# Kernel optimization log

Hardware: AMD Instinct MI355X
Metric: run time of the kernel (lower is better)

The kernel has to match this reference:

```python
import jax, jax.numpy as jnp
import numpy as np

N = 100000      # nodes
E = 1600000     # edges (before self-loops)
IN_C = 128
HID = 256
L = 4
EPS = 1e-5


def setup_inputs() -> dict:
    key = jax.random.key(0)
    ks = jax.random.split(key, 12)
    s = 0.05
    x = jax.random.normal(ks[0], (N, IN_C), dtype=jnp.float32)
    edge_index = jax.random.randint(ks[1], (2, E), 0, N, dtype=jnp.int64)
    enc_w = jax.random.normal(ks[2], (IN_C, HID), dtype=jnp.float32) * s
    enc_b = jnp.zeros((HID,), jnp.float32)
    conv_w = jax.random.normal(ks[3], (L, HID, HID), dtype=jnp.float32) * s
    conv_b = jnp.zeros((L, HID), jnp.float32)
    ln_g = jnp.ones((L, HID), jnp.float32)
    ln_b = jnp.zeros((L, HID), jnp.float32)
    lin1_w = jax.random.normal(ks[4], (HID, HID // 2), dtype=jnp.float32) * s
    lin1_b = jnp.zeros((HID // 2,), jnp.float32)
    lin2_w = jax.random.normal(ks[5], (HID // 2, 1), dtype=jnp.float32) * s
    lin2_b = jnp.zeros((1,), jnp.float32)
    return dict(x=x, edge_index=edge_index, enc_w=enc_w, enc_b=enc_b,
                conv_w=conv_w, conv_b=conv_b, ln_g=ln_g, ln_b=ln_b,
                lin1_w=lin1_w, lin1_b=lin1_b, lin2_w=lin2_w, lin2_b=lin2_b)


def _layer_norm(h, g, b):
    mu = jnp.mean(h, axis=-1, keepdims=True)
    var = jnp.mean(jnp.square(h - mu), axis=-1, keepdims=True)
    return (h - mu) * jax.lax.rsqrt(var + EPS) * g + b


def reference(x, edge_index, enc_w, enc_b, conv_w, conv_b, ln_g, ln_b,
              lin1_w, lin1_b, lin2_w, lin2_b):
    loops = jnp.arange(N, dtype=edge_index.dtype)
    row = jnp.concatenate([edge_index[0], loops])   # source
    col = jnp.concatenate([edge_index[1], loops])   # target
    # GCN symmetric norm with self-loop weight 1 (improved=False)
    deg = jax.ops.segment_sum(jnp.ones(row.shape[0], jnp.float32), col,
                              num_segments=N)
    dis = jnp.where(deg > 0, jax.lax.rsqrt(deg), 0.0)  # deg^-1/2, [N]

    h = x @ enc_w + enc_b
    for i in range(L):
        hw = h @ conv_w[i]
        # norm_e = dis[row]*dis[col]: scale at source, aggregate, scale at target
        agg = jax.ops.segment_sum((hw * dis[:, None])[row], col,
                                  num_segments=N)
        h = agg * dis[:, None] + conv_b[i]
        h = jax.nn.relu(_layer_norm(h, ln_g[i], ln_b[i]))
        # dropout p=0.1 is identity in eval mode
    h = jax.nn.relu(h @ lin1_w + lin1_b)
    return h @ lin2_w + lin2_b  # [N, 1]
```

## Files before the change

### kernel.cpp

```cpp
#include <hip/hip_runtime.h>

#define N_NODES 100000
#define N_EDGES 1600000
#define IN_C    128
#define HID     256
#define NLAYER  4

#define NBUCK 391
#define BCAP  8192
#define EPB   4096
#define CAPL  6144

typedef __attribute__((ext_vector_type(8))) __bf16 bf16x8;
typedef __attribute__((ext_vector_type(4))) float  floatx4;

__device__ inline unsigned short f2b(float f) {
    unsigned u = __builtin_bit_cast(unsigned, f);
    return (unsigned short)((u + 0x7fffu + ((u >> 16) & 1u)) >> 16);
}
__device__ inline float b2f(unsigned short s) {
    unsigned u = ((unsigned)s) << 16;
    return __builtin_bit_cast(float, u);
}
__device__ inline void acc8(float* a, uint4 v) {
    unsigned wds[4] = {v.x, v.y, v.z, v.w};
    #pragma unroll
    for (int k = 0; k < 4; ++k) {
        a[2*k]   += __builtin_bit_cast(float, wds[k] << 16);
        a[2*k+1] += __builtin_bit_cast(float, wds[k] & 0xffff0000u);
    }
}

__global__ void kb_zero(int* g, int m) {
    int i = blockIdx.x * blockDim.x + threadIdx.x;
    if (i < m) g[i] = 0;
}

__global__ __launch_bounds__(256) void kb_scatter(
        const int* __restrict__ row, const int* __restrict__ col,
        int* __restrict__ gfill, uint2* __restrict__ pairs, int e) {
    __shared__ uint2 ep[EPB];
    __shared__ int hist[NBUCK];
    __shared__ int lbase[NBUCK];
    const int tid  = threadIdx.x;
    const int base = blockIdx.x * EPB;
    for (int b = tid; b < NBUCK; b += 256) hist[b] = 0;
    __syncthreads();
    #pragma unroll
    for (int k = 0; k < EPB / 256; ++k) {
        int i = base + k * 256 + tid;
        uint2 pr = make_uint2(0xffffffffu, 0u);
        if (i < e) {
            pr.x = (unsigned)col[i];
            pr.y = (unsigned)row[i];
            atomicAdd(&hist[pr.x >> 8], 1);
        }
        ep[k * 256 + tid] = pr;
    }
    __syncthreads();
    for (int b = tid; b < NBUCK; b += 256) {
        int h = hist[b];
        lbase[b] = h ? atomicAdd(&gfill[b], h) : 0;
    }
    __syncthreads();
    for (int b = tid; b < NBUCK; b += 256) hist[b] = 0;
    __syncthreads();
    #pragma unroll
    for (int k = 0; k < EPB / 256; ++k) {
        uint2 pr = ep[k * 256 + tid];
        if (pr.x != 0xffffffffu) {
            int bk = pr.x >> 8;
            int p  = lbase[bk] + atomicAdd(&hist[bk], 1);
            if (p < BCAP) pairs[(size_t)bk * BCAP + p] = pr;
        }
    }
}

__global__ void kb_scan(const int* __restrict__ gfill, int* __restrict__ boff,
                        int* __restrict__ offs) {
    __shared__ int wsum[8];
    const int t = threadIdx.x, lane = t & 63, w = t >> 6;
    int v = (t < NBUCK) ? gfill[t] : 0;
    int inc = v;
    #pragma unroll
    for (int o = 1; o < 64; o <<= 1) { int u = __shfl_up(inc, o); if (lane >= o) inc += u; }
    if (lane == 63) wsum[w] = inc;
    __syncthreads();
    if (t == 0) { int r = 0; for (int i = 0; i < 8; ++i) { int x = wsum[i]; wsum[i] = r; r += x; } }
    __syncthreads();
    int excl = wsum[w] + inc - v;
    if (t <= NBUCK) boff[t] = excl;
    if (t == 0) offs[N_NODES] = N_EDGES;
}

__global__ __launch_bounds__(256) void kb_build(
        const uint2* __restrict__ pairs, const int* __restrict__ gfill,
        const int* __restrict__ boff,
        int* __restrict__ offs, float* __restrict__ dis,
        int* __restrict__ srcl, int n) {
    __shared__ int lcnt[256];
    __shared__ int lstart[256];
    __shared__ int wsum[4];
    __shared__ int sl[CAPL];
    const int b = blockIdx.x;
    const int tid = threadIdx.x, lane = tid & 63, w = tid >> 6;
    int cnt = gfill[b]; if (cnt > CAPL) cnt = CAPL;
    const int base = boff[b];
    const uint2* bp = pairs + (size_t)b * BCAP;
    lcnt[tid] = 0;
    __syncthreads();
    for (int i = tid; i < cnt; i += 256)
        atomicAdd(&lcnt[bp[i].x & 255], 1);
    __syncthreads();
    int v = lcnt[tid];
    int inc = v;
    #pragma unroll
    for (int o = 1; o < 64; o <<= 1) { int u = __shfl_up(inc, o); if (lane >= o) inc += u; }
    if (lane == 63) wsum[w] = inc;
    __syncthreads();
    if (tid == 0) { int r = 0; for (int i = 0; i < 4; ++i) { int x = wsum[i]; wsum[i] = r; r += x; } }
    __syncthreads();
    int excl = wsum[w] + inc - v;
    lstart[tid] = excl;
    int node = (b << 8) + tid;
    if (node < n) {
        dis[node]  = rsqrtf((float)(v + 1));
        offs[node] = base + excl;
    }
    __syncthreads();
    lcnt[tid] = 0;
    __syncthreads();
    for (int i = tid; i < cnt; i += 256) {
        uint2 pr = bp[i];
        int c = pr.x & 255;
        int q = lstart[c] + atomicAdd(&lcnt[c], 1);
        sl[q] = (int)pr.y;
    }
    __syncthreads();
    for (int i = tid; i < cnt; i += 256)
        srcl[base + i] = sl[i];
}

__global__ void k_f2b4(const float* __restrict__ src, unsigned short* __restrict__ dst, int n4) {
    int i = blockIdx.x * blockDim.x + threadIdx.x;
    if (i < n4) {
        float4 v = ((const float4*)src)[i];
        ushort4 o;
        o.x = f2b(v.x); o.y = f2b(v.y); o.z = f2b(v.z); o.w = f2b(v.w);
        ((ushort4*)dst)[i] = o;
    }
}

__global__ void k_wt(const float* __restrict__ W, unsigned short* __restrict__ Wt, int K, int Nn) {
    int idx = blockIdx.x * blockDim.x + threadIdx.x;
    if (idx < K * Nn) {
        int k = idx / Nn, n = idx % Nn;
        Wt[n * K + k] = f2b(W[idx]);
    }
}

template<int MODE>
__global__ __launch_bounds__(256) void k_mm(
        const unsigned short* __restrict__ A,
        const unsigned short* __restrict__ Wt,
        const float* __restrict__ bias, const float* __restrict__ scale,
        void* __restrict__ Cout, int M, int K, int Nn) {
    __shared__ unsigned short As[128 * 32];
    __shared__ unsigned short Bs[128 * 32];
    const int tid  = threadIdx.x;
    const int lane = tid & 63;
    const int w    = tid >> 6;
    const int bm   = blockIdx.x * 128;
    const int bn   = blockIdx.y * 128;

    const int i0 = tid, i1 = tid + 256;
    const int r0 = i0 >> 2, r1 = i1 >> 2;
    const int q0 = i0 & 3,  q1 = i1 & 3;
    const int a_off0 = min(bm + r0, M - 1) * K + q0 * 8;
    const int a_off1 = min(bm + r1, M - 1) * K + q1 * 8;
    const int b_off0 = (bn + r0) * K + q0 * 8;
    const int b_off1 = (bn + r1) * K + q1 * 8;

    uint4 ra0, ra1, rb0, rb1;
    floatx4 acc[4][4];
    #pragma unroll
    for (int i = 0; i < 4; ++i)
        #pragma unroll
        for (int j = 0; j < 4; ++j)
            acc[i][j] = (floatx4){0.f, 0.f, 0.f, 0.f};

    const int wm = (w & 1) * 64;
    const int wn = (w >> 1) * 64;
    const int fm = lane & 15;
    const int fq = (lane >> 4) * 8;

    ra0 = *(const uint4*)(A  + a_off0);
    ra1 = *(const uint4*)(A  + a_off1);
    rb0 = *(const uint4*)(Wt + b_off0);
    rb1 = *(const uint4*)(Wt + b_off1);

    const int KT = K >> 5;
    for (int kt = 0; kt < KT; ++kt) {
        ((uint4*)As)[i0] = ra0; ((uint4*)As)[i1] = ra1;
        ((uint4*)Bs)[i0] = rb0; ((uint4*)Bs)[i1] = rb1;
        __syncthreads();
        if (kt + 1 < KT) {
            int k0 = (kt + 1) << 5;
            ra0 = *(const uint4*)(A  + a_off0 + k0);
            ra1 = *(const uint4*)(A  + a_off1 + k0);
            rb0 = *(const uint4*)(Wt + b_off0 + k0);
            rb1 = *(const uint4*)(Wt + b_off1 + k0);
        }
        bf16x8 af[4], bfr[4];
        #pragma unroll
        for (int i = 0; i < 4; ++i)
            af[i] = *(const bf16x8*)(const void*)(As + (wm + i * 16 + fm) * 32 + fq);
        #pragma unroll
        for (int j = 0; j < 4; ++j)
            bfr[j] = *(const bf16x8*)(const void*)(Bs + (wn + j * 16 + fm) * 32 + fq);
        #pragma unroll
        for (int i = 0; i < 4; ++i)
            #pragma unroll
            for (int j = 0; j < 4; ++j)
                acc[i][j] = __builtin_amdgcn_mfma_f32_16x16x32_bf16(af[i], bfr[j], acc[i][j], 0, 0, 0);
        __syncthreads();
    }

    const int quad = lane >> 4;
    #pragma unroll
    for (int i = 0; i < 4; ++i) {
        #pragma unroll
        for (int r = 0; r < 4; ++r) {
            int row = bm + wm + i * 16 + quad * 4 + r;
            if (row >= M) continue;
            float sc = scale ? scale[row] : 1.f;
            #pragma unroll
            for (int j = 0; j < 4; ++j) {
                int colg = bn + wn + j * 16 + fm;
                float v = acc[i][j][r];
                if (MODE == 0) v += bias[colg];
                v *= sc;
                ((unsigned short*)Cout)[(size_t)row * Nn + colg] = f2b(v);
            }
        }
    }
}

__global__ __launch_bounds__(256) void k_head(
        const unsigned short* __restrict__ A,
        const unsigned short* __restrict__ Wt,
        const float* __restrict__ b1, const float* __restrict__ w2,
        const float* __restrict__ b2, float* __restrict__ out, int M) {
    const int K = 256;
    __shared__ unsigned short As[128 * 32];
    __shared__ unsigned short Bs[128 * 32];
    const int tid  = threadIdx.x;
    const int lane = tid & 63;
    const int w    = tid >> 6;
    const int bm   = blockIdx.x * 128;

    const int i0 = tid, i1 = tid + 256;
    const int r0 = i0 >> 2, r1 = i1 >> 2;
    const int q0 = i0 & 3,  q1 = i1 & 3;
    const int a_off0 = min(bm + r0, M - 1) * K + q0 * 8;
    const int a_off1 = min(bm + r1, M - 1) * K + q1 * 8;
    const int b_off0 = r0 * K + q0 * 8;
    const int b_off1 = r1 * K + q1 * 8;

    uint4 ra0, ra1, rb0, rb1;
    floatx4 acc[4][4];
    #pragma unroll
    for (int i = 0; i < 4; ++i)
        #pragma unroll
        for (int j = 0; j < 4; ++j)
            acc[i][j] = (floatx4){0.f, 0.f, 0.f, 0.f};

    const int wm = (w & 1) * 64;
    const int wn = (w >> 1) * 64;
    const int fm = lane & 15;
    const int fq = (lane >> 4) * 8;

    ra0 = *(const uint4*)(A  + a_off0);
    ra1 = *(const uint4*)(A  + a_off1);
    rb0 = *(const uint4*)(Wt + b_off0);
    rb1 = *(const uint4*)(Wt + b_off1);

    for (int kt = 0; kt < 8; ++kt) {
        ((uint4*)As)[i0] = ra0; ((uint4*)As)[i1] = ra1;
        ((uint4*)Bs)[i0] = rb0; ((uint4*)Bs)[i1] = rb1;
        __syncthreads();
        if (kt + 1 < 8) {
            int k0 = (kt + 1) << 5;
            ra0 = *(const uint4*)(A  + a_off0 + k0);
            ra1 = *(const uint4*)(A  + a_off1 + k0);
            rb0 = *(const uint4*)(Wt + b_off0 + k0);
            rb1 = *(const uint4*)(Wt + b_off1 + k0);
        }
        bf16x8 af[4], bfr[4];
        #pragma unroll
        for (int i = 0; i < 4; ++i)
            af[i] = *(const bf16x8*)(const void*)(As + (wm + i * 16 + fm) * 32 + fq);
        #pragma unroll
        for (int j = 0; j < 4; ++j)
            bfr[j] = *(const bf16x8*)(const void*)(Bs + (wn + j * 16 + fm) * 32 + fq);
        #pragma unroll
        for (int i = 0; i < 4; ++i)
            #pragma unroll
            for (int j = 0; j < 4; ++j)
                acc[i][j] = __builtin_amdgcn_mfma_f32_16x16x32_bf16(af[i], bfr[j], acc[i][j], 0, 0, 0);
        __syncthreads();
    }

    float* red = (float*)As;
    const int q = lane >> 4;
    float b1v[4], w2v[4];
    #pragma unroll
    for (int j = 0; j < 4; ++j) {
        int col = wn + j * 16 + fm;
        b1v[j] = b1[col]; w2v[j] = w2[col];
    }
    #pragma unroll
    for (int i = 0; i < 4; ++i) {
        #pragma unroll
        for (int r = 0; r < 4; ++r) {
            float s = 0.f;
            #pragma unroll
            for (int j = 0; j < 4; ++j)
                s += fmaxf(acc[i][j][r] + b1v[j], 0.f) * w2v[j];
            #pragma unroll
            for (int off = 1; off < 16; off <<= 1) s += __shfl_xor(s, off);
            if (fm == 0) {
                int m = wm + i * 16 + q * 4 + r;
                red[m * 2 + (wn >> 6)] = s;
            }
        }
    }
    __syncthreads();
    if (tid < 128) {
        int row = bm + tid;
        if (row < M) out[row] = red[tid * 2] + red[tid * 2 + 1] + b2[0];
    }
}

__global__ void k_agg(const unsigned short* __restrict__ hw, const int* __restrict__ srcl,
                      const int* __restrict__ offs, const float* __restrict__ dis,
                      const float* __restrict__ cb, const float* __restrict__ g,
                      const float* __restrict__ bt, unsigned short* __restrict__ hout, int n) {
    int gtid = blockIdx.x * blockDim.x + threadIdx.x;
    int node = __builtin_amdgcn_readfirstlane(gtid >> 6);
    int lane = threadIdx.x & 63;
    const int half = lane >> 5;
    const int sub  = lane & 31;
    const uint4* T = (const uint4*)hw;

    float a[8] = {0,0,0,0,0,0,0,0};
    float c[8] = {0,0,0,0,0,0,0,0};
    if (half == 0) {
        uint4 v = T[(size_t)node * 32 + sub];
        acc8(a, v);
    }
    int p = offs[node], pe = offs[node + 1];
    for (; p + 7 < pe; p += 8) {
        int s0 = srcl[p],     s1 = srcl[p + 1], s2 = srcl[p + 2], s3 = srcl[p + 3];
        int s4 = srcl[p + 4], s5 = srcl[p + 5], s6 = srcl[p + 6], s7 = srcl[p + 7];
        int ea = half ? s1 : s0;
        int eb = half ? s3 : s2;
        int ec = half ? s5 : s4;
        int ed = half ? s7 : s6;
        uint4 va = T[(size_t)ea * 32 + sub];
        uint4 vb = T[(size_t)eb * 32 + sub];
        uint4 vc = T[(size_t)ec * 32 + sub];
        uint4 vd = T[(size_t)ed * 32 + sub];
        acc8(a, va);
        acc8(c, vb);
        acc8(a, vc);
        acc8(c, vd);
    }
    for (; p + 1 < pe; p += 2) {
        int s0 = srcl[p], s1 = srcl[p + 1];
        int ea = half ? s1 : s0;
        uint4 v = T[(size_t)ea * 32 + sub];
        acc8(a, v);
    }
    if (p < pe && half == 0) {
        int s0 = srcl[p];
        uint4 v = T[(size_t)s0 * 32 + sub];
        acc8(a, v);
    }
    #pragma unroll
    for (int j = 0; j < 8; ++j) {
        a[j] += c[j];
        a[j] += __shfl_xor(a[j], 32);
    }
    float dc = dis[node];
    const float4* cb4 = (const float4*)cb;
    const float4* g4  = (const float4*)g;
    const float4* bt4 = (const float4*)bt;
    float4 cba = cb4[sub * 2], cbb = cb4[sub * 2 + 1];
    float h[8];
    h[0] = fmaf(a[0], dc, cba.x); h[1] = fmaf(a[1], dc, cba.y);
    h[2] = fmaf(a[2], dc, cba.z); h[3] = fmaf(a[3], dc, cba.w);
    h[4] = fmaf(a[4], dc, cbb.x); h[5] = fmaf(a[5], dc, cbb.y);
    h[6] = fmaf(a[6], dc, cbb.z); h[7] = fmaf(a[7], dc, cbb.w);
    float s = 0.f, sq = 0.f;
    #pragma unroll
    for (int j = 0; j < 8; ++j) { s += h[j]; sq += h[j] * h[j]; }
    #pragma unroll
    for (int off = 1; off < 32; off <<= 1) { s += __shfl_xor(s, off); sq += __shfl_xor(sq, off); }
    float mu  = s * (1.f / 256.f);
    float var = sq * (1.f / 256.f) - mu * mu;
    float inv = rsqrtf(var + 1e-5f);
    if (half == 0) {
        float4 ga = g4[sub * 2], gb = g4[sub * 2 + 1];
        float4 ba = bt4[sub * 2], bb = bt4[sub * 2 + 1];
        float gv[8] = {ga.x, ga.y, ga.z, ga.w, gb.x, gb.y, gb.z, gb.w};
        float bv[8] = {ba.x, ba.y, ba.z, ba.w, bb.x, bb.y, bb.z, bb.w};
        unsigned short o[8];
        #pragma unroll
        for (int j = 0; j < 8; ++j)
            o[j] = f2b(fmaxf(fmaf((h[j] - mu) * inv, gv[j], bv[j]), 0.f));
        uint4 st;
        st.x = (unsigned)o[0] | ((unsigned)o[1] << 16);
        st.y = (unsigned)o[2] | ((unsigned)o[3] << 16);
        st.z = (unsigned)o[4] | ((unsigned)o[5] << 16);
        st.w = (unsigned)o[6] | ((unsigned)o[7] << 16);
        ((uint4*)hout)[(size_t)node * 32 + sub] = st;
    }
}

extern "C" void kernel_launch(void* const* d_in, const int* in_sizes, int n_in,
                              void* d_out, int out_size, void* d_ws, size_t ws_size,
                              hipStream_t stream) {
    const float* x      = (const float*)d_in[0];
    const int*   ei     = (const int*)d_in[1];
    const float* enc_w  = (const float*)d_in[2];
    const float* enc_b  = (const float*)d_in[3];
    const float* conv_w = (const float*)d_in[4];
    const float* conv_b = (const float*)d_in[5];
    const float* ln_g   = (const float*)d_in[6];
    const float* ln_b   = (const float*)d_in[7];
    const float* w1     = (const float*)d_in[8];
    const float* b1     = (const float*)d_in[9];
    const float* w2     = (const float*)d_in[10];
    const float* b2     = (const float*)d_in[11];
    float* out = (float*)d_out;

    char* ws = (char*)d_ws;
    size_t off = 0;
    auto alloc = [&](size_t bytes) -> void* {
        void* p = ws + off;
        off = (off + bytes + 255) & ~(size_t)255;
        return p;
    };
    int*   offs  = (int*)alloc((size_t)(N_NODES + 1) * 4);
    int*   srcl  = (int*)alloc((size_t)N_EDGES * 4);
    float* dis   = (float*)alloc((size_t)N_NODES * 4);
    int*   gfill = (int*)alloc((size_t)NBUCK * 4);
    int*   boff  = (int*)alloc((size_t)(NBUCK + 1) * 4);
    unsigned short* hb = (unsigned short*)alloc((size_t)N_NODES * HID * 2);
    unsigned short* hw = (unsigned short*)alloc((size_t)N_NODES * HID * 2);
    size_t pairs_bytes = (size_t)NBUCK * BCAP * 8;
    size_t xb_bytes    = (size_t)N_NODES * IN_C * 2;
    char* R3 = (char*)alloc(pairs_bytes > xb_bytes ? pairs_bytes : xb_bytes);
    uint2*          pairs = (uint2*)R3;
    unsigned short* xb    = (unsigned short*)R3;
    unsigned short* enc_t  = (unsigned short*)alloc((size_t)IN_C * HID * 2);
    unsigned short* conv_t = (unsigned short*)alloc((size_t)NLAYER * HID * HID * 2);
    unsigned short* lin1_t = (unsigned short*)alloc((size_t)HID * (HID / 2) * 2);

    const int* row = ei;
    const int* col = ei + N_EDGES;

    kb_zero<<<(NBUCK + 255) / 256, 256, 0, stream>>>(gfill, NBUCK);
    kb_scatter<<<(N_EDGES + EPB - 1) / EPB, 256, 0, stream>>>(row, col, gfill, pairs, N_EDGES);
    kb_scan<<<1, 512, 0, stream>>>(gfill, boff, offs);
    kb_build<<<NBUCK, 256, 0, stream>>>(pairs, gfill, boff, offs, dis, srcl, N_NODES);

    int xn4 = N_NODES * IN_C / 4;
    k_f2b4<<<(xn4 + 255) / 256, 256, 0, stream>>>(x, xb, xn4);
    k_wt<<<(IN_C * HID + 255) / 256, 256, 0, stream>>>(enc_w, enc_t, IN_C, HID);
    for (int l = 0; l < NLAYER; ++l)
        k_wt<<<(HID * HID + 255) / 256, 256, 0, stream>>>(
            conv_w + (size_t)l * HID * HID, conv_t + (size_t)l * HID * HID, HID, HID);
    k_wt<<<(HID * (HID / 2) + 255) / 256, 256, 0, stream>>>(w1, lin1_t, HID, HID / 2);

    {
        dim3 g((N_NODES + 127) / 128, HID / 128);
        k_mm<0><<<g, 256, 0, stream>>>(xb, enc_t, enc_b, nullptr, hb, N_NODES, IN_C, HID);
    }

    for (int l = 0; l < NLAYER; ++l) {
        dim3 g((N_NODES + 127) / 128, HID / 128);
        k_mm<1><<<g, 256, 0, stream>>>(hb, conv_t + (size_t)l * HID * HID, nullptr, dis,
                                       hw, N_NODES, HID, HID);
        k_agg<<<(N_NODES * 64 + 255) / 256, 256, 0, stream>>>(
            hw, srcl, offs, dis, conv_b + l * HID, ln_g + l * HID, ln_b + l * HID, hb, N_NODES);
    }

    k_head<<<(N_NODES + 127) / 128, 256, 0, stream>>>(hb, lin1_t, b1, w2, b2, out, N_NODES);
}
```

Before: 833.2 us.

## Fuse fp32-to-bf16 conversion into encoder GEMM, merge weight prep, deepen aggregation unroll

The encoder GEMM now reads fp32 x directly and converts to bf16 while loading, which removes the separate conversion kernel and its intermediate buffer. The six weight-transpose launches are merged into one kernel. The aggregation loop gains a 16-edge unrolled stage so more gathers are in flight, and accumulation uses packed float2 vectors to encourage packed FP32 adds. In exchange the encoder reads twice the bytes for x (fp32 instead of bf16) and both GEMM column blocks redo the conversion, and the deeper unroll raises register pressure.

```diff
diff --git a/kernel.cpp b/kernel.cpp
--- a/kernel.cpp
+++ b/kernel.cpp
@@ -13,21 +13,20 @@
 
 typedef __attribute__((ext_vector_type(8))) __bf16 bf16x8;
 typedef __attribute__((ext_vector_type(4))) float  floatx4;
+typedef __attribute__((ext_vector_type(2))) float  floatx2;
 
 __device__ inline unsigned short f2b(float f) {
     unsigned u = __builtin_bit_cast(unsigned, f);
     return (unsigned short)((u + 0x7fffu + ((u >> 16) & 1u)) >> 16);
 }
-__device__ inline float b2f(unsigned short s) {
-    unsigned u = ((unsigned)s) << 16;
-    return __builtin_bit_cast(float, u);
-}
-__device__ inline void acc8(float* a, uint4 v) {
+__device__ inline void acc8p(floatx2* a, uint4 v) {
     unsigned wds[4] = {v.x, v.y, v.z, v.w};
     #pragma unroll
     for (int k = 0; k < 4; ++k) {
-        a[2*k]   += __builtin_bit_cast(float, wds[k] << 16);
-        a[2*k+1] += __builtin_bit_cast(float, wds[k] & 0xffff0000u);
+        floatx2 t;
+        t.x = __builtin_bit_cast(float, wds[k] << 16);
+        t.y = __builtin_bit_cast(float, wds[k] & 0xffff0000u);
+        a[k] += t;
     }
 }
 
@@ -141,27 +140,30 @@
         srcl[base + i] = sl[i];
 }
 
-__global__ void k_f2b4(const float* __restrict__ src, unsigned short* __restrict__ dst, int n4) {
-    int i = blockIdx.x * blockDim.x + threadIdx.x;
-    if (i < n4) {
-        float4 v = ((const float4*)src)[i];
-        ushort4 o;
-        o.x = f2b(v.x); o.y = f2b(v.y); o.z = f2b(v.z); o.w = f2b(v.w);
-        ((ushort4*)dst)[i] = o;
-    }
-}
-
-__global__ void k_wt(const float* __restrict__ W, unsigned short* __restrict__ Wt, int K, int Nn) {
+__global__ void k_wt_all(const float* __restrict__ enc_w, const float* __restrict__ conv_w,
+                         const float* __restrict__ w1,
+                         unsigned short* __restrict__ enc_t, unsigned short* __restrict__ conv_t,
+                         unsigned short* __restrict__ lin1_t) {
     int idx = blockIdx.x * blockDim.x + threadIdx.x;
-    if (idx < K * Nn) {
-        int k = idx / Nn, n = idx % Nn;
-        Wt[n * K + k] = f2b(W[idx]);
+    if (idx < IN_C * HID) {
+        int k = idx / HID, n = idx % HID;
+        enc_t[n * IN_C + k] = f2b(enc_w[idx]);
+    } else if (idx < IN_C * HID + NLAYER * HID * HID) {
+        int r = idx - IN_C * HID;
+        int l = r / (HID * HID);
+        int e = r % (HID * HID);
+        int k = e / HID, n = e % HID;
+        conv_t[(size_t)l * HID * HID + n * HID + k] = f2b(conv_w[r]);
+    } else if (idx < IN_C * HID + NLAYER * HID * HID + HID * (HID / 2)) {
+        int e = idx - (IN_C * HID + NLAYER * HID * HID);
+        int k = e / (HID / 2), n = e % (HID / 2);
+        lin1_t[n * HID + k] = f2b(w1[e]);
     }
 }
 
 template<int MODE>
 __global__ __launch_bounds__(256) void k_mm(
-        const unsigned short* __restrict__ A,
+        const void* __restrict__ Ain,
         const unsigned short* __restrict__ Wt,
         const float* __restrict__ bias, const float* __restrict__ scale,
         void* __restrict__ Cout, int M, int K, int Nn) {
@@ -181,7 +183,6 @@
     const int b_off0 = (bn + r0) * K + q0 * 8;
     const int b_off1 = (bn + r1) * K + q1 * 8;
 
-    uint4 ra0, ra1, rb0, rb1;
     floatx4 acc[4][4];
     #pragma unroll
     for (int i = 0; i < 4; ++i)
@@ -194,8 +195,31 @@
     const int fm = lane & 15;
     const int fq = (lane >> 4) * 8;
 
-    ra0 = *(const uint4*)(A  + a_off0);
-    ra1 = *(const uint4*)(A  + a_off1);
+    const unsigned short* Ab = (const unsigned short*)Ain;
+    const float*          Af = (const float*)Ain;
+
+    uint4 ra0, ra1, rb0, rb1;
+    auto loadA = [&](int koff, uint4& oa0, uint4& oa1) {
+        if (MODE == 0) {
+            float4 f0 = *(const float4*)(Af + a_off0 + koff);
+            float4 f1 = *(const float4*)(Af + a_off0 + koff + 4);
+            oa0.x = (unsigned)f2b(f0.x) | ((unsigned)f2b(f0.y) << 16);
+            oa0.y = (unsigned)f2b(f0.z) | ((unsigned)f2b(f0.w) << 16);
+            oa0.z = (unsigned)f2b(f1.x) | ((unsigned)f2b(f1.y) << 16);
+            oa0.w = (unsigned)f2b(f1.z) | ((unsigned)f2b(f1.w) << 16);
+            float4 g0 = *(const float4*)(Af + a_off1 + koff);
+            float4 g1 = *(const float4*)(Af + a_off1 + koff + 4);
+            oa1.x = (unsigned)f2b(g0.x) | ((unsigned)f2b(g0.y) << 16);
+            oa1.y = (unsigned)f2b(g0.z) | ((unsigned)f2b(g0.w) << 16);
+            oa1.z = (unsigned)f2b(g1.x) | ((unsigned)f2b(g1.y) << 16);
+            oa1.w = (unsigned)f2b(g1.z) | ((unsigned)f2b(g1.w) << 16);
+        } else {
+            oa0 = *(const uint4*)(Ab + a_off0 + koff);
+            oa1 = *(const uint4*)(Ab + a_off1 + koff);
+        }
+    };
+
+    loadA(0, ra0, ra1);
     rb0 = *(const uint4*)(Wt + b_off0);
     rb1 = *(const uint4*)(Wt + b_off1);
 
@@ -206,8 +230,7 @@
         __syncthreads();
         if (kt + 1 < KT) {
             int k0 = (kt + 1) << 5;
-            ra0 = *(const uint4*)(A  + a_off0 + k0);
-            ra1 = *(const uint4*)(A  + a_off1 + k0);
+            loadA(k0, ra0, ra1);
             rb0 = *(const uint4*)(Wt + b_off0 + k0);
             rb1 = *(const uint4*)(Wt + b_off1 + k0);
         }
@@ -280,8 +303,8 @@
     const int fm = lane & 15;
     const int fq = (lane >> 4) * 8;
 
-    ra0 = *(const uint4*)(A  + a_off0);
-    ra1 = *(const uint4*)(A  + a_off1);
+    ra0 = *(const uint4*)(A + a_off0);
+    ra1 = *(const uint4*)(A + a_off1);
     rb0 = *(const uint4*)(Wt + b_off0);
     rb1 = *(const uint4*)(Wt + b_off1);
 
@@ -291,8 +314,8 @@
         __syncthreads();
         if (kt + 1 < 8) {
             int k0 = (kt + 1) << 5;
-            ra0 = *(const uint4*)(A  + a_off0 + k0);
-            ra1 = *(const uint4*)(A  + a_off1 + k0);
+            ra0 = *(const uint4*)(A + a_off0 + k0);
+            ra1 = *(const uint4*)(A + a_off1 + k0);
             rb0 = *(const uint4*)(Wt + b_off0 + k0);
             rb1 = *(const uint4*)(Wt + b_off1 + k0);
         }
@@ -353,44 +376,53 @@
     const int sub  = lane & 31;
     const uint4* T = (const uint4*)hw;
 
-    float a[8] = {0,0,0,0,0,0,0,0};
-    float c[8] = {0,0,0,0,0,0,0,0};
+    floatx2 A0[4], C0[4];
+    #pragma unroll
+    for (int k = 0; k < 4; ++k) { A0[k] = (floatx2){0.f, 0.f}; C0[k] = (floatx2){0.f, 0.f}; }
     if (half == 0) {
         uint4 v = T[(size_t)node * 32 + sub];
-        acc8(a, v);
+        acc8p(A0, v);
     }
     int p = offs[node], pe = offs[node + 1];
+    for (; p + 15 < pe; p += 16) {
+        int s[16];
+        #pragma unroll
+        for (int t = 0; t < 16; ++t) s[t] = srcl[p + t];
+        uint4 v0 = T[(size_t)(half ? s[1]  : s[0])  * 32 + sub];
+        uint4 v1 = T[(size_t)(half ? s[3]  : s[2])  * 32 + sub];
+        uint4 v2 = T[(size_t)(half ? s[5]  : s[4])  * 32 + sub];
+        uint4 v3 = T[(size_t)(half ? s[7]  : s[6])  * 32 + sub];
+        uint4 v4 = T[(size_t)(half ? s[9]  : s[8])  * 32 + sub];
+        uint4 v5 = T[(size_t)(half ? s[11] : s[10]) * 32 + sub];
+        uint4 v6 = T[(size_t)(half ? s[13] : s[12]) * 32 + sub];
+        uint4 v7 = T[(size_t)(half ? s[15] : s[14]) * 32 + sub];
+        acc8p(A0, v0); acc8p(C0, v1); acc8p(A0, v2); acc8p(C0, v3);
+        acc8p(A0, v4); acc8p(C0, v5); acc8p(A0, v6); acc8p(C0, v7);
+    }
     for (; p + 7 < pe; p += 8) {
         int s0 = srcl[p],     s1 = srcl[p + 1], s2 = srcl[p + 2], s3 = srcl[p + 3];
         int s4 = srcl[p + 4], s5 = srcl[p + 5], s6 = srcl[p + 6], s7 = srcl[p + 7];
-        int ea = half ? s1 : s0;
-        int eb = half ? s3 : s2;
-        int ec = half ? s5 : s4;
-        int ed = half ? s7 : s6;
-        uint4 va = T[(size_t)ea * 32 + sub];
-        uint4 vb = T[(size_t)eb * 32 + sub];
-        uint4 vc = T[(size_t)ec * 32 + sub];
-        uint4 vd = T[(size_t)ed * 32 + sub];
-        acc8(a, va);
-        acc8(c, vb);
-        acc8(a, vc);
-        acc8(c, vd);
+        uint4 v0 = T[(size_t)(half ? s1 : s0) * 32 + sub];
+        uint4 v1 = T[(size_t)(half ? s3 : s2) * 32 + sub];
+        uint4 v2 = T[(size_t)(half ? s5 : s4) * 32 + sub];
+        uint4 v3 = T[(size_t)(half ? s7 : s6) * 32 + sub];
+        acc8p(A0, v0); acc8p(C0, v1); acc8p(A0, v2); acc8p(C0, v3);
     }
     for (; p + 1 < pe; p += 2) {
         int s0 = srcl[p], s1 = srcl[p + 1];
-        int ea = half ? s1 : s0;
-        uint4 v = T[(size_t)ea * 32 + sub];
-        acc8(a, v);
+        uint4 v = T[(size_t)(half ? s1 : s0) * 32 + sub];
+        acc8p(A0, v);
     }
     if (p < pe && half == 0) {
-        int s0 = srcl[p];
-        uint4 v = T[(size_t)s0 * 32 + sub];
-        acc8(a, v);
-    }
-    #pragma unroll
-    for (int j = 0; j < 8; ++j) {
-        a[j] += c[j];
-        a[j] += __shfl_xor(a[j], 32);
+        uint4 v = T[(size_t)srcl[p] * 32 + sub];
+        acc8p(A0, v);
+    }
+    float a[8];
+    #pragma unroll
+    for (int k = 0; k < 4; ++k) {
+        floatx2 t = A0[k] + C0[k];
+        a[2 * k]     = t.x + __shfl_xor(t.x, 32);
+        a[2 * k + 1] = t.y + __shfl_xor(t.y, 32);
     }
     float dc = dis[node];
     const float4* cb4 = (const float4*)cb;
@@ -459,11 +491,7 @@
     int*   boff  = (int*)alloc((size_t)(NBUCK + 1) * 4);
     unsigned short* hb = (unsigned short*)alloc((size_t)N_NODES * HID * 2);
     unsigned short* hw = (unsigned short*)alloc((size_t)N_NODES * HID * 2);
-    size_t pairs_bytes = (size_t)NBUCK * BCAP * 8;
-    size_t xb_bytes    = (size_t)N_NODES * IN_C * 2;
-    char* R3 = (char*)alloc(pairs_bytes > xb_bytes ? pairs_bytes : xb_bytes);
-    uint2*          pairs = (uint2*)R3;
-    unsigned short* xb    = (unsigned short*)R3;
+    uint2* pairs = (uint2*)alloc((size_t)NBUCK * BCAP * 8);
     unsigned short* enc_t  = (unsigned short*)alloc((size_t)IN_C * HID * 2);
     unsigned short* conv_t = (unsigned short*)alloc((size_t)NLAYER * HID * HID * 2);
     unsigned short* lin1_t = (unsigned short*)alloc((size_t)HID * (HID / 2) * 2);
@@ -476,17 +504,14 @@
     kb_scan<<<1, 512, 0, stream>>>(gfill, boff, offs);
     kb_build<<<NBUCK, 256, 0, stream>>>(pairs, gfill, boff, offs, dis, srcl, N_NODES);
 
-    int xn4 = N_NODES * IN_C / 4;
-    k_f2b4<<<(xn4 + 255) / 256, 256, 0, stream>>>(x, xb, xn4);
-    k_wt<<<(IN_C * HID + 255) / 256, 256, 0, stream>>>(enc_w, enc_t, IN_C, HID);
-    for (int l = 0; l < NLAYER; ++l)
-        k_wt<<<(HID * HID + 255) / 256, 256, 0, stream>>>(
-            conv_w + (size_t)l * HID * HID, conv_t + (size_t)l * HID * HID, HID, HID);
-    k_wt<<<(HID * (HID / 2) + 255) / 256, 256, 0, stream>>>(w1, lin1_t, HID, HID / 2);
+    {
+        int tot = IN_C * HID + NLAYER * HID * HID + HID * (HID / 2);
+        k_wt_all<<<(tot + 255) / 256, 256, 0, stream>>>(enc_w, conv_w, w1, enc_t, conv_t, lin1_t);
+    }
 
     {
         dim3 g((N_NODES + 127) / 128, HID / 128);
-        k_mm<0><<<g, 256, 0, stream>>>(xb, enc_t, enc_b, nullptr, hb, N_NODES, IN_C, HID);
+        k_mm<0><<<g, 256, 0, stream>>>(x, enc_t, enc_b, nullptr, hb, N_NODES, IN_C, HID);
     }
 
     for (int l = 0; l < NLAYER; ++l) {
```

Measured after the change: 827.2 us. About the same (-0.7%).
